# Kernel optimization log

Hardware: AMD Instinct MI355X
Metric: run time of the kernel (lower is better)

Reference implementation:

```python
import jax, jax.numpy as jnp
import numpy as np

B, C, D, H, W = 8, 1, 160, 160, 160
SPATIAL_AXES = (2, 3, 4)  # axial, coronal, sagittal map to dims D, H, W


def setup_inputs() -> dict:
    key = jax.random.key(0)
    k1, _ = jax.random.split(key)
    x = jax.random.normal(k1, (B, C, D, H, W), dtype=jnp.float32)
    log_sigma = jnp.zeros((3,), dtype=jnp.float32)  # log(initial_sigma=1.0)
    return {"x": x, "log_sigma": log_sigma}


def reference(x, log_sigma):
    # For each spatial axis: adjacent-slice diff, squared distance summed over
    # channel + remaining spatial dims (per batch, per slice-pair), RBF kernel,
    # then -mean over (batch, slice-pairs). Equivalent to the original
    # sum_i(-mean_b(k_i)) / (n_slices - 1) since mean is linear.
    sigma = jnp.exp(log_sigma)
    total = jnp.float32(0.0)
    for i, ax in enumerate(SPATIAL_AXES):
        d = jnp.diff(x, axis=ax)  # [B, C, ...] with S-1 along ax
        reduce_dims = tuple(a for a in range(5) if a not in (0, ax))
        sq = jnp.sum(d * d, axis=reduce_dims)  # [B, S-1]
        k = jnp.exp(-sq / (2.0 * sigma[i] ** 2))
        total = total + (-jnp.mean(k))
    return total / jnp.float32(len(SPATIAL_AXES))
```

## Files before the change

kernel.cpp:

```cpp
#include <hip/hip_runtime.h>


constexpr int Wd4 = 40;
constexpr int SLICE4 = 6400;
constexpr long BSTR4 = 160L * 6400;
constexpr int NB = 8;
constexpr int NPAIR = 159;
constexpr int PBATCH = NB * NPAIR;
constexpr int NKEY = 3 * PBATCH;
constexpr int NBLK = NB * 160;
constexpr int NRED = 60;
constexpr int HT_OFF = 5 * PBATCH;
constexpr int WT_OFF = 37 * PBATCH;

__device__ __forceinline__ float sq4(const float4& a, const float4& c) {
    float e0 = a.x - c.x, e1 = a.y - c.y, e2 = a.z - c.z, e3 = a.w - c.w;
    return e0 * e0 + e1 * e1 + e2 * e2 + e3 * e3;
}

__global__ __launch_bounds__(320) void diff3_kernel(const float* __restrict__ x,
                                                    float* __restrict__ ws,
                                                    float* __restrict__ out) {
    __shared__ float lds[1504];

    const int t = threadIdx.x;
    const int bid = blockIdx.x;
    const int b = bid / 160;
    const int r2 = bid % 160;
    const int ds = r2 / 5;
    const int hc = r2 % 5;
    const int d0 = ds * 5, h0 = hc * 32;
    const bool lastSeg = (ds == 31);

    const int c4 = t % 40;
    const int rp = t / 40;
    const int lane = t & 63;
    const int wv = t >> 6;
    const bool hOK = !(hc == 4 && rp == 7);
    const bool sOK = (c4 < 39);
    const bool fixB = (lane == 63) && sOK;

    if (bid == 0 && t == 0) out[0] = 0.f;

    const float4* base = (const float4*)x + (size_t)b * BSTR4 + (size_t)d0 * SLICE4
                       + (size_t)(h0 + 4 * rp) * Wd4 + c4;

    float aW[4] = {0.f, 0.f, 0.f, 0.f};
    float aH[4] = {0.f, 0.f, 0.f, 0.f};
    float aD[5] = {0.f, 0.f, 0.f, 0.f, 0.f};
    float4 p0, p1, p2, p3;

#pragma unroll
    for (int it = 0; it < 5; ++it) {
        const float4* sp = base + it * SLICE4;
        const float4 v0 = sp[0];
        const float4 v1 = sp[Wd4];
        const float4 v2 = sp[2 * Wd4];
        const float4 v3 = sp[3 * Wd4];
        float4 hv;
        if (hOK) hv = sp[4 * Wd4];
        float bx0 = 0.f, bx1 = 0.f, bx2 = 0.f, bx3 = 0.f;
        if (fixB) {
            bx0 = ((const float*)(sp))[4];
            bx1 = ((const float*)(sp + Wd4))[4];
            bx2 = ((const float*)(sp + 2 * Wd4))[4];
            bx3 = ((const float*)(sp + 3 * Wd4))[4];
        }
        float s0 = __shfl_down(v0.x, 1, 64); if (fixB) s0 = bx0;
        float s1 = __shfl_down(v1.x, 1, 64); if (fixB) s1 = bx1;
        float s2 = __shfl_down(v2.x, 1, 64); if (fixB) s2 = bx2;
        float s3 = __shfl_down(v3.x, 1, 64); if (fixB) s3 = bx3;

        float dw;
        dw = v0.y - v0.x; aW[0] += dw * dw;
        dw = v0.z - v0.y; aW[1] += dw * dw;
        dw = v0.w - v0.z; aW[2] += dw * dw;
        dw = v1.y - v1.x; aW[0] += dw * dw;
        dw = v1.z - v1.y; aW[1] += dw * dw;
        dw = v1.w - v1.z; aW[2] += dw * dw;
        dw = v2.y - v2.x; aW[0] += dw * dw;
        dw = v2.z - v2.y; aW[1] += dw * dw;
        dw = v2.w - v2.z; aW[2] += dw * dw;
        dw = v3.y - v3.x; aW[0] += dw * dw;
        dw = v3.z - v3.y; aW[1] += dw * dw;
        dw = v3.w - v3.z; aW[2] += dw * dw;
        if (sOK) {
            dw = s0 - v0.w; aW[3] += dw * dw;
            dw = s1 - v1.w; aW[3] += dw * dw;
            dw = s2 - v2.w; aW[3] += dw * dw;
            dw = s3 - v3.w; aW[3] += dw * dw;
        }
        aH[0] += sq4(v1, v0);
        aH[1] += sq4(v2, v1);
        aH[2] += sq4(v3, v2);
        if (hOK) aH[3] += sq4(hv, v3);
        if (it > 0)
            aD[it - 1] += sq4(v0, p0) + sq4(v1, p1) + sq4(v2, p2) + sq4(v3, p3);
        p0 = v0; p1 = v1; p2 = v2; p3 = v3;
    }
    if (!lastSeg) {
        const float4* sp = base + 5 * SLICE4;
        aD[4] = sq4(sp[0], p0) + sq4(sp[Wd4], p1) + sq4(sp[2 * Wd4], p2) + sq4(sp[3 * Wd4], p3);
    }

#pragma unroll
    for (int j = 0; j < 4; ++j) lds[(4 * rp + j) * 41 + c4] = aH[j];
#pragma unroll
    for (int j = 0; j < 5; ++j) {
        float dd = aD[j];
        for (int off = 32; off > 0; off >>= 1) dd += __shfl_down(dd, off, 64);
        if (lane == 0) lds[1472 + j * 5 + wv] = dd;
    }
    __syncthreads();
    float hsum = 0.f, dsum = 0.f;
    if (t < 32) {
        const float* src = &lds[t * 41];
        for (int i = 0; i < 40; ++i) hsum += src[i];
    }
    if (t < 5) {
        for (int w2 = 0; w2 < 5; ++w2) dsum += lds[1472 + t * 5 + w2];
    }
    __syncthreads();
#pragma unroll
    for (int j = 0; j < 4; ++j) lds[(4 * c4 + j) * 9 + rp] = aW[j];
    __syncthreads();
    float wsum = 0.f;
    if (t < 160) {
        const float* src = &lds[t * 9];
        for (int i = 0; i < 8; ++i) wsum += src[i];
    }

    const int kb = b * NPAIR;
    if (t < 5 && (d0 + t) < NPAIR)  ws[hc * PBATCH + kb + d0 + t] = dsum;
    if (t < 32 && (h0 + t) < NPAIR) ws[HT_OFF + ds * PBATCH + kb + h0 + t] = hsum;
    if (t < NPAIR)                  ws[WT_OFF + r2 * PBATCH + kb + t] = wsum;
}

__global__ __launch_bounds__(64) void reduce_kernel(const float* __restrict__ ws,
                                                    const float* __restrict__ log_sigma,
                                                    float* __restrict__ out) {
    const int gk = blockIdx.x * 64 + threadIdx.x;
    float kv = 0.f;
    if (gk < NKEY) {
        const int a = gk / PBATCH;
        const int rem = gk % PBATCH;
        const float f = -0.5f * expf(-2.f * log_sigma[a]);
        float val = 0.f;
        if (a == 0) {
            for (int hc = 0; hc < 5; ++hc)   val += ws[hc * PBATCH + rem];
        } else if (a == 1) {
            for (int dss = 0; dss < 32; ++dss) val += ws[HT_OFF + dss * PBATCH + rem];
        } else {
            for (int ci = 0; ci < 160; ++ci) val += ws[WT_OFF + ci * PBATCH + rem];
        }
        kv = expf(val * f);
    }
    for (int off = 32; off > 0; off >>= 1) kv += __shfl_down(kv, off, 64);
    if (threadIdx.x == 0) atomicAdd(out, -kv / (float)NKEY);
}

extern "C" void kernel_launch(void* const* d_in, const int* in_sizes, int n_in,
                              void* d_out, int out_size, void* d_ws, size_t ws_size,
                              hipStream_t stream) {
    const float* x = (const float*)d_in[0];
    const float* log_sigma = (const float*)d_in[1];
    float* out = (float*)d_out;
    float* ws = (float*)d_ws;

    diff3_kernel<<<NBLK, 320, 0, stream>>>(x, ws, out);
    reduce_kernel<<<NRED, 64, 0, stream>>>(ws, log_sigma, out);
}
```

Measured before the change: 197.0 us.

## Add coalesced cache-warming pass with soft grid barrier before diff computation

Before the real work, each block streams one full contiguous slice of the input with perfectly coalesced float4 loads and throws the sums away, so the whole volume gets pulled into the large last-level cache. The block then joins a bounded-spin grid barrier on an atomic counter, which a new tiny kernel zeroes along with the output. The main strided diff pass is meant to hit cache instead of HBM, and a launch-bounds occupancy hint is added so all blocks can be resident at once. The cost is reading the input twice, plus a spin wait and an extra kernel launch.

```diff
diff --git a/kernel.cpp b/kernel.cpp
--- a/kernel.cpp
+++ b/kernel.cpp
@@ -12,19 +12,50 @@
 constexpr int NRED = 60;
 constexpr int HT_OFF = 5 * PBATCH;
 constexpr int WT_OFF = 37 * PBATCH;
+constexpr int CNT_OFF = 197 * PBATCH;
 
 __device__ __forceinline__ float sq4(const float4& a, const float4& c) {
     float e0 = a.x - c.x, e1 = a.y - c.y, e2 = a.z - c.z, e3 = a.w - c.w;
     return e0 * e0 + e1 * e1 + e2 * e2 + e3 * e3;
 }
 
-__global__ __launch_bounds__(320) void diff3_kernel(const float* __restrict__ x,
-                                                    float* __restrict__ ws,
-                                                    float* __restrict__ out) {
+__global__ __launch_bounds__(64) void zero_kernel(float* __restrict__ ws,
+                                                  float* __restrict__ out) {
+    if (threadIdx.x == 0) {
+        *(int*)(ws + CNT_OFF) = 0;
+        out[0] = 0.f;
+    }
+}
+
+__global__ __launch_bounds__(320, 7) void diff3_kernel(const float* __restrict__ x,
+                                                       float* __restrict__ ws) {
     __shared__ float lds[1504];
 
     const int t = threadIdx.x;
     const int bid = blockIdx.x;
+
+    {
+        const float4* sp = (const float4*)x + (size_t)bid * SLICE4;
+        float s0 = 0.f, s1 = 0.f, s2 = 0.f, s3 = 0.f;
+#pragma unroll
+        for (int r = 0; r < 20; ++r) {
+            const float4 v = sp[r * 320 + t];
+            s0 += v.x; s1 += v.y; s2 += v.z; s3 += v.w;
+        }
+        asm volatile("" :: "v"(s0), "v"(s1), "v"(s2), "v"(s3));
+        if (t == 0) {
+            int* cnt = (int*)(ws + CNT_OFF);
+            __hip_atomic_fetch_add(cnt, 1, __ATOMIC_RELAXED, __HIP_MEMORY_SCOPE_AGENT);
+            int spins = 0;
+            while (__hip_atomic_load(cnt, __ATOMIC_RELAXED, __HIP_MEMORY_SCOPE_AGENT) < NBLK
+                   && spins < 128) {
+                __builtin_amdgcn_s_sleep(32);
+                ++spins;
+            }
+        }
+        __syncthreads();
+    }
+
     const int b = bid / 160;
     const int r2 = bid % 160;
     const int ds = r2 / 5;
@@ -39,8 +70,6 @@
     const bool hOK = !(hc == 4 && rp == 7);
     const bool sOK = (c4 < 39);
     const bool fixB = (lane == 63) && sOK;
-
-    if (bid == 0 && t == 0) out[0] = 0.f;
 
     const float4* base = (const float4*)x + (size_t)b * BSTR4 + (size_t)d0 * SLICE4
                        + (size_t)(h0 + 4 * rp) * Wd4 + c4;
@@ -167,6 +196,7 @@
     float* out = (float*)d_out;
     float* ws = (float*)d_ws;
 
-    diff3_kernel<<<NBLK, 320, 0, stream>>>(x, ws, out);
+    zero_kernel<<<1, 64, 0, stream>>>(ws, out);
+    diff3_kernel<<<NBLK, 320, 0, stream>>>(x, ws);
     reduce_kernel<<<NRED, 64, 0, stream>>>(ws, log_sigma, out);
 }
```

New measurement: 319.2 us. 1.62x slower.
